# Kernel optimization log

Hardware: AMD Instinct MI355X
Metric: run time of the kernel (lower is better)

The kernel has to match this reference:

```python
import jax, jax.numpy as jnp
import numpy as np

TEMPERATURE = 0.1
GAMMA = 0.5
LOSS_WEIGHT = 1.0
N, D = 8192, 64
EPS_COS = 1e-8
EPS_NCE = 1e-6
SQ_EPS = 1e-12  # (1e-6 distance)^2


def setup_inputs() -> dict:
    key = jax.random.key(0)
    k1, k2, k3 = jax.random.split(key, 3)
    features = jax.random.normal(k1, (N, D), dtype=jnp.float32)
    labels = jax.random.randint(k2, (N,), 0, 3, dtype=jnp.int64)
    coords = jax.random.uniform(k3, (N, 3), dtype=jnp.float32)
    return {"features": features, "labels": labels, "coords": coords}


def reference(features, labels, coords):
    # line-point mask (label == 2); pairwise math on the masked subset is
    # expressed as full pairwise + (m_i & m_j) masking, mathematically
    # identical to extract-then-pairwise in the torch original.
    m = labels == 2                       # [N] bool
    mf = m.astype(features.dtype)
    L = jnp.sum(mf)                       # number of line points

    # cosine similarity: normalize then GEMM (== F.cosine_similarity pairwise)
    norm = jnp.maximum(jnp.linalg.norm(features, axis=1, keepdims=True), EPS_COS)
    fn = features / norm
    feat_sim = fn @ fn.T                  # [N, N]

    # squared pairwise coordinate distances (cdist^2), clamped >= 0
    sq_norm = jnp.sum(coords * coords, axis=1)
    sq = sq_norm[:, None] + sq_norm[None, :] - 2.0 * (coords @ coords.T)
    sq = jnp.maximum(sq, 0.0)             # [N, N]

    pair = m[:, None] & m[None, :]
    within = (sq < 1.0) & (sq > SQ_EPS)   # dist < 1.0 and dist > 1e-6
    pos = pair & within
    neg = pair & ~within                  # original neg_mask = ~pos over subset

    posf = pos.astype(feat_sim.dtype)
    negf = neg.astype(feat_sim.dtype)

    exp_sim = jnp.exp(feat_sim / TEMPERATURE)
    sum_exp = jnp.sum(exp_sim * negf, axis=1)
    pos_sum = jnp.sum(exp_sim * posf, axis=1)
    ratio = pos_sum / (sum_exp + pos_sum + EPS_NCE)
    # mean of -log(ratio) over line points only (guard non-line rows)
    per_point = -jnp.log(jnp.where(m, ratio, 1.0))
    info_nce = jnp.sum(per_point * mf) / L

    # continuity: mean over the L x L subset matrix of |(1 - sim) - dist| * pos
    safe_sq = jnp.where(pos, sq, 1.0)     # avoid sqrt(0) NaN grads on masked entries
    coord_dist = jnp.sqrt(safe_sq)
    continuity = jnp.sum(jnp.abs((1.0 - feat_sim) - coord_dist) * posf) / (L * L)

    return (info_nce + GAMMA * continuity) * LOSS_WEIGHT
```

## Files before the change

### kernel.cpp

```cpp
#include <hip/hip_runtime.h>
#include <math.h>


typedef short s16x8 __attribute__((ext_vector_type(8)));
typedef float f32x4 __attribute__((ext_vector_type(4)));

#define NPTS 8192
#define DIM 64
#define BT 128
#define GRID_P 512
#define PSTRIDE 4096
#define MAXSLOT 32

#define OFF_L 0
#define OFF_IDX 1024
#define OFF_FH (OFF_IDX + NPTS * 4)
#define OFF_FL (OFF_FH + NPTS * DIM * 2)
#define OFF_CS (OFF_FL + NPTS * DIM * 2)
#define OFF_DF (OFF_CS + NPTS * 16)
#define OFF_PP (OFF_DF + NPTS * 4)
#define OFF_PN (OFF_PP + MAXSLOT * PSTRIDE * 4)
#define OFF_CT (OFF_PN + MAXSLOT * PSTRIDE * 4)

__global__ __launch_bounds__(1024) void k_scan(const int* __restrict__ labels,
                                               int* __restrict__ idx,
                                               int* __restrict__ Lout) {
  __shared__ int wres[16];
  __shared__ int wsum[16];
  const int t = threadIdx.x;
  const int lane = t & 63;
  const int wid = t >> 6;
  const int base = t * 8;
  int w[8];
#pragma unroll
  for (int j = 0; j < 8; j++) w[j] = labels[base + j];
  int oddz = (w[1] == 0) && (w[3] == 0) && (w[5] == 0) && (w[7] == 0);
  unsigned long long wa = __ballot(!oddz);
  if (lane == 0) wres[wid] = (wa == 0ull);
  __syncthreads();
  int is64 = 1;
#pragma unroll
  for (int i = 0; i < 16; i++) is64 &= wres[i];

  int bits = 0, cnt = 0;
  if (is64) {
    const long long* l64 = (const long long*)labels;
#pragma unroll
    for (int j = 0; j < 8; j++) {
      bool f = (l64[base + j] == 2ll);
      bits |= ((int)f) << j;
      cnt += (int)f;
    }
  } else {
#pragma unroll
    for (int j = 0; j < 8; j++) {
      bool f = (w[j] == 2);
      bits |= ((int)f) << j;
      cnt += (int)f;
    }
  }
  int inc = cnt;
#pragma unroll
  for (int m = 1; m < 64; m <<= 1) {
    int v = __shfl_up(inc, m);
    if (lane >= m) inc += v;
  }
  if (lane == 63) wsum[wid] = inc;
  __syncthreads();
  if (t < 16) {
    int v = wsum[t];
    int sc = v;
#pragma unroll
    for (int m = 1; m < 16; m <<= 1) {
      int u = __shfl_up(sc, m);
      if (t >= m) sc += u;
    }
    wsum[t] = sc - v;
    if (t == 15) *Lout = sc;
  }
  __syncthreads();
  int pos = wsum[wid] + inc - cnt;
#pragma unroll
  for (int j = 0; j < 8; j++) {
    if (bits & (1 << j)) idx[pos++] = base + j;
  }
}

__global__ __launch_bounds__(256) void k_gather(const float* __restrict__ feats,
                                                const float* __restrict__ coords,
                                                const int* __restrict__ idx,
                                                const int* __restrict__ Lp,
                                                ushort* __restrict__ fnHi,
                                                ushort* __restrict__ fnLo,
                                                float4* __restrict__ cs,
                                                int* __restrict__ diagf) {
  const int L = *Lp;
  const int gw = (int)((blockIdx.x * blockDim.x + threadIdx.x) >> 6);
  const int lane = threadIdx.x & 63;
  if (gw >= L) {
    fnHi[gw * 64 + lane] = 0;
    fnLo[gw * 64 + lane] = 0;
    if (lane == 0) {
      cs[gw] = make_float4(0.f, 0.f, 0.f, 0.f);
      diagf[gw] = 0;
    }
    return;
  }
  const int row = idx[gw];
  float f = feats[row * DIM + lane];
  float ss = f * f;
#pragma unroll
  for (int m = 32; m; m >>= 1) ss += __shfl_xor(ss, m);
  float nrm = fmaxf(sqrtf(ss), 1e-8f);
  float fn = f / nrm;
  unsigned u = __float_as_uint(fn);
  unsigned hb = (u + 0x7FFFu + ((u >> 16) & 1u)) >> 16;
  float hif = __uint_as_float(hb << 16);
  float lof = fn - hif;
  unsigned ul = __float_as_uint(lof);
  unsigned lb = (ul + 0x7FFFu + ((ul >> 16) & 1u)) >> 16;
  fnHi[gw * 64 + lane] = (ushort)hb;
  fnLo[gw * 64 + lane] = (ushort)lb;
  if (lane == 0) {
    float c0 = coords[row * 3 + 0];
    float c1 = coords[row * 3 + 1];
    float c2 = coords[row * 3 + 2];
    float p0 = __fmul_rn(c0, c0);
    float p1 = __fmul_rn(c1, c1);
    float p2 = __fmul_rn(c2, c2);
    float s = __fadd_rn(__fadd_rn(p0, p1), p2);
    float g = __fadd_rn(__fadd_rn(p0, p2), p1);
    diagf[gw] = (__fadd_rn(s, -g) > 5e-13f) ? 1 : 0;
    cs[gw] = make_float4(c0, c1, c2, c0 * c0 + c1 * c1 + c2 * c2);
  }
}

__global__ __launch_bounds__(256, 3) void k_pair(const ushort* __restrict__ fnHi,
                                                 const ushort* __restrict__ fnLo,
                                                 const float4* __restrict__ cs,
                                                 const int* __restrict__ Lp,
                                                 const int* __restrict__ diagf,
                                                 float* __restrict__ pp,
                                                 float* __restrict__ pn,
                                                 float* __restrict__ contp) {
  __shared__ __attribute__((aligned(16))) ushort AB[4][128][40];
  __shared__ float cred[4];

  const int L = *Lp;
  const int nT = (L + BT - 1) >> 7;
  const int nItems = nT * nT;
  const int t = threadIdx.x;
  const int lane = t & 63, wid = t >> 6;
  const int m = lane & 15;
  const int koct = lane >> 4;
  float cont = 0.f;

  for (int wi = blockIdx.x; wi < nItems; wi += GRID_P) {
    const int bi = wi / nT;
    const int jt = wi - bi * nT;
    const bool isDiag = (bi == jt);
    const int rb = bi << 7, cb = jt << 7;

    f32x4 acc[2][8];
#pragma unroll
    for (int rt = 0; rt < 2; rt++)
#pragma unroll
      for (int ct = 0; ct < 8; ct++) acc[rt][ct] = (f32x4){0.f, 0.f, 0.f, 0.f};

#pragma unroll
    for (int kk = 0; kk < 2; kk++) {
      __syncthreads();
#pragma unroll
      for (int i = 0; i < 8; i++) {
        int q = t + 256 * i;
        int sel = q >> 9;
        int row = (q >> 2) & 127;
        int oct = q & 3;
        int slot = ((sel < 2) ? rb : cb) + row;
        const ushort* src = (sel & 1) ? fnLo : fnHi;
        s16x8 v = *(const s16x8*)&src[slot * 64 + kk * 32 + oct * 8];
        *(s16x8*)&AB[sel][row][oct * 8] = v;
      }
      __syncthreads();

      const int kofd = koct * 8;
      s16x8 ah[2], al[2], bh[8], bl[8];
#pragma unroll
      for (int rt = 0; rt < 2; rt++) {
        ah[rt] = *(const s16x8*)&AB[0][wid * 32 + rt * 16 + m][kofd];
        al[rt] = *(const s16x8*)&AB[1][wid * 32 + rt * 16 + m][kofd];
      }
#pragma unroll
      for (int ct = 0; ct < 8; ct++) {
        bh[ct] = *(const s16x8*)&AB[2][ct * 16 + m][kofd];
        bl[ct] = *(const s16x8*)&AB[3][ct * 16 + m][kofd];
      }
#pragma unroll
      for (int rt = 0; rt < 2; rt++)
#pragma unroll
        for (int ct = 0; ct < 8; ct++) {
          acc[rt][ct] = __builtin_amdgcn_mfma_f32_16x16x32_bf16(ah[rt], bh[ct], acc[rt][ct], 0, 0, 0);
          acc[rt][ct] = __builtin_amdgcn_mfma_f32_16x16x32_bf16(ah[rt], bl[ct], acc[rt][ct], 0, 0, 0);
          acc[rt][ct] = __builtin_amdgcn_mfma_f32_16x16x32_bf16(al[rt], bh[ct], acc[rt][ct], 0, 0, 0);
        }
    }

    float4 crow[2][4];
    int dfr[2][4];
#pragma unroll
    for (int rt = 0; rt < 2; rt++)
#pragma unroll
      for (int rg = 0; rg < 4; rg++) {
        int ig = rb + wid * 32 + rt * 16 + koct * 4 + rg;
        crow[rt][rg] = cs[ig];
        dfr[rt][rg] = isDiag ? diagf[ig] : 0;
      }
    float pos_r[2][4] = {{0.f, 0.f, 0.f, 0.f}, {0.f, 0.f, 0.f, 0.f}};
    float neg_r[2][4] = {{0.f, 0.f, 0.f, 0.f}, {0.f, 0.f, 0.f, 0.f}};
#pragma unroll
    for (int ct = 0; ct < 8; ct++) {
      int jg = cb + ct * 16 + m;
      float4 cbv = cs[jg];
      bool jv = (jg < L);
#pragma unroll
      for (int rt = 0; rt < 2; rt++)
#pragma unroll
        for (int rg = 0; rg < 4; rg++) {
          int ig = rb + wid * 32 + rt * 16 + koct * 4 + rg;
          bool valid = jv && (ig < L);
          float sim = acc[rt][ct][rg];
          float4 cav = crow[rt][rg];
          float d3 = cav.x * cbv.x + cav.y * cbv.y + cav.z * cbv.z;
          float sq = fmaxf(cav.w + cbv.w - 2.f * d3, 0.f);
          bool within = (sq < 1.0f) && (sq > 1e-12f);
          if (isDiag && ig == jg) within = (dfr[rt][rg] != 0);
          float e = __expf(sim * 10.f);
          if (valid) {
            if (within) {
              pos_r[rt][rg] += e;
              cont += fabsf(1.f - sim - sqrtf(sq));
            } else {
              neg_r[rt][rg] += e;
            }
          }
        }
    }
#pragma unroll
    for (int rt = 0; rt < 2; rt++)
#pragma unroll
      for (int rg = 0; rg < 4; rg++) {
        float p = pos_r[rt][rg], n = neg_r[rt][rg];
#pragma unroll
        for (int s1 = 1; s1 < 16; s1 <<= 1) {
          p += __shfl_xor(p, s1);
          n += __shfl_xor(n, s1);
        }
        if (m == 0) {
          int ig = rb + wid * 32 + rt * 16 + koct * 4 + rg;
          pp[jt * PSTRIDE + ig] = p;
          pn[jt * PSTRIDE + ig] = n;
        }
      }
  }

#pragma unroll
  for (int s1 = 1; s1 < 64; s1 <<= 1) cont += __shfl_xor(cont, s1);
  __syncthreads();
  if (lane == 0) cred[wid] = cont;
  __syncthreads();
  if (t == 0) contp[blockIdx.x] = cred[0] + cred[1] + cred[2] + cred[3];
}

__global__ __launch_bounds__(1024) void k_final(const float* __restrict__ pp,
                                                const float* __restrict__ pn,
                                                const float* __restrict__ contp,
                                                const int* __restrict__ Lp,
                                                float* __restrict__ out) {
  __shared__ float red[32];
  const int L = *Lp;
  const int nslots = (L + BT - 1) >> 7;
  const int t = threadIdx.x;
  float accI = 0.f;
  for (int s = t; s < L; s += 1024) {
    float pos = 0.f, neg = 0.f;
    for (int c = 0; c < nslots; c++) {
      pos += pp[c * PSTRIDE + s];
      neg += pn[c * PSTRIDE + s];
    }
    accI += -logf(pos / (neg + pos + 1e-6f));
  }
  float accC = 0.f;
  for (int c = t; c < GRID_P; c += 1024) accC += contp[c];
#pragma unroll
  for (int m = 1; m < 64; m <<= 1) {
    accI += __shfl_xor(accI, m);
    accC += __shfl_xor(accC, m);
  }
  if ((t & 63) == 0) {
    red[t >> 6] = accI;
    red[16 + (t >> 6)] = accC;
  }
  __syncthreads();
  if (t == 0) {
    float sI = 0.f, sC = 0.f;
#pragma unroll
    for (int w = 0; w < 16; w++) {
      sI += red[w];
      sC += red[16 + w];
    }
    float fL = (float)L;
    out[0] = sI / fL + 0.5f * (sC / (fL * fL));
  }
}

extern "C" void kernel_launch(void* const* d_in, const int* in_sizes, int n_in,
                              void* d_out, int out_size, void* d_ws, size_t ws_size,
                              hipStream_t stream) {
  const float* features = (const float*)d_in[0];
  const int* labels = (const int*)d_in[1];
  const float* coords = (const float*)d_in[2];

  char* ws = (char*)d_ws;
  int* Lp = (int*)(ws + OFF_L);
  int* idx = (int*)(ws + OFF_IDX);
  ushort* fnHi = (ushort*)(ws + OFF_FH);
  ushort* fnLo = (ushort*)(ws + OFF_FL);
  float4* cs = (float4*)(ws + OFF_CS);
  int* diagf = (int*)(ws + OFF_DF);
  float* pp = (float*)(ws + OFF_PP);
  float* pn = (float*)(ws + OFF_PN);
  float* contp = (float*)(ws + OFF_CT);
  float* out = (float*)d_out;

  k_scan<<<1, 1024, 0, stream>>>(labels, idx, Lp);
  k_gather<<<(NPTS * 64) / 256, 256, 0, stream>>>(features, coords, idx, Lp, fnHi, fnLo, cs, diagf);
  k_pair<<<GRID_P, 256, 0, stream>>>(fnHi, fnLo, cs, Lp, diagf, pp, pn, contp);
  k_final<<<1, 1024, 0, stream>>>(pp, pn, contp, Lp, out);
}
```

Before: 49.84 us.

## Fuse label scan and feature gather into one multi-block prep kernel

Merges the single-block label compaction scan and the per-row normalize/split gather into one kernel. Each of 64 blocks redundantly recomputes the prefix scan into shared memory and then gathers its share of rows, which removes a kernel launch and the global index buffer. In exchange, the scan is redundant across blocks and uses a barrier-heavy shared-memory Hillis-Steele loop. The gather also runs with far fewer blocks, and padding now stops at the next multiple of 128 rather than covering all rows.

```diff
diff --git a/kernel.cpp b/kernel.cpp
--- a/kernel.cpp
+++ b/kernel.cpp
@@ -13,8 +13,7 @@
 #define MAXSLOT 32
 
 #define OFF_L 0
-#define OFF_IDX 1024
-#define OFF_FH (OFF_IDX + NPTS * 4)
+#define OFF_FH 1024
 #define OFF_FL (OFF_FH + NPTS * DIM * 2)
 #define OFF_CS (OFF_FL + NPTS * DIM * 2)
 #define OFF_DF (OFF_CS + NPTS * 16)
@@ -22,15 +21,22 @@
 #define OFF_PN (OFF_PP + MAXSLOT * PSTRIDE * 4)
 #define OFF_CT (OFF_PN + MAXSLOT * PSTRIDE * 4)
 
-__global__ __launch_bounds__(1024) void k_scan(const int* __restrict__ labels,
-                                               int* __restrict__ idx,
-                                               int* __restrict__ Lout) {
+__global__ __launch_bounds__(1024) void k_prep(const float* __restrict__ feats,
+                                               const int* __restrict__ labels,
+                                               const float* __restrict__ coords,
+                                               int* __restrict__ Lp,
+                                               ushort* __restrict__ fnHi,
+                                               ushort* __restrict__ fnLo,
+                                               float4* __restrict__ cs,
+                                               int* __restrict__ diagf) {
+  __shared__ int sc[1024];
+  __shared__ int sidx[NPTS];
   __shared__ int wres[16];
-  __shared__ int wsum[16];
   const int t = threadIdx.x;
   const int lane = t & 63;
   const int wid = t >> 6;
   const int base = t * 8;
+
   int w[8];
 #pragma unroll
   for (int j = 0; j < 8; j++) w[j] = labels[base + j];
@@ -59,79 +65,62 @@
       cnt += (int)f;
     }
   }
-  int inc = cnt;
-#pragma unroll
-  for (int m = 1; m < 64; m <<= 1) {
-    int v = __shfl_up(inc, m);
-    if (lane >= m) inc += v;
-  }
-  if (lane == 63) wsum[wid] = inc;
-  __syncthreads();
-  if (t < 16) {
-    int v = wsum[t];
-    int sc = v;
-#pragma unroll
-    for (int m = 1; m < 16; m <<= 1) {
-      int u = __shfl_up(sc, m);
-      if (t >= m) sc += u;
-    }
-    wsum[t] = sc - v;
-    if (t == 15) *Lout = sc;
-  }
-  __syncthreads();
-  int pos = wsum[wid] + inc - cnt;
+  sc[t] = cnt;
+  __syncthreads();
+  for (int off = 1; off < 1024; off <<= 1) {
+    int v = 0;
+    if (t >= off) v = sc[t - off];
+    __syncthreads();
+    sc[t] += v;
+    __syncthreads();
+  }
+  int pos = sc[t] - cnt;
 #pragma unroll
   for (int j = 0; j < 8; j++) {
-    if (bits & (1 << j)) idx[pos++] = base + j;
-  }
-}
-
-__global__ __launch_bounds__(256) void k_gather(const float* __restrict__ feats,
-                                                const float* __restrict__ coords,
-                                                const int* __restrict__ idx,
-                                                const int* __restrict__ Lp,
-                                                ushort* __restrict__ fnHi,
-                                                ushort* __restrict__ fnLo,
-                                                float4* __restrict__ cs,
-                                                int* __restrict__ diagf) {
-  const int L = *Lp;
-  const int gw = (int)((blockIdx.x * blockDim.x + threadIdx.x) >> 6);
-  const int lane = threadIdx.x & 63;
-  if (gw >= L) {
-    fnHi[gw * 64 + lane] = 0;
-    fnLo[gw * 64 + lane] = 0;
-    if (lane == 0) {
-      cs[gw] = make_float4(0.f, 0.f, 0.f, 0.f);
-      diagf[gw] = 0;
-    }
-    return;
-  }
-  const int row = idx[gw];
-  float f = feats[row * DIM + lane];
-  float ss = f * f;
-#pragma unroll
-  for (int m = 32; m; m >>= 1) ss += __shfl_xor(ss, m);
-  float nrm = fmaxf(sqrtf(ss), 1e-8f);
-  float fn = f / nrm;
-  unsigned u = __float_as_uint(fn);
-  unsigned hb = (u + 0x7FFFu + ((u >> 16) & 1u)) >> 16;
-  float hif = __uint_as_float(hb << 16);
-  float lof = fn - hif;
-  unsigned ul = __float_as_uint(lof);
-  unsigned lb = (ul + 0x7FFFu + ((ul >> 16) & 1u)) >> 16;
-  fnHi[gw * 64 + lane] = (ushort)hb;
-  fnLo[gw * 64 + lane] = (ushort)lb;
-  if (lane == 0) {
-    float c0 = coords[row * 3 + 0];
-    float c1 = coords[row * 3 + 1];
-    float c2 = coords[row * 3 + 2];
-    float p0 = __fmul_rn(c0, c0);
-    float p1 = __fmul_rn(c1, c1);
-    float p2 = __fmul_rn(c2, c2);
-    float s = __fadd_rn(__fadd_rn(p0, p1), p2);
-    float g = __fadd_rn(__fadd_rn(p0, p2), p1);
-    diagf[gw] = (__fadd_rn(s, -g) > 5e-13f) ? 1 : 0;
-    cs[gw] = make_float4(c0, c1, c2, c0 * c0 + c1 * c1 + c2 * c2);
+    if (bits & (1 << j)) sidx[pos++] = base + j;
+  }
+  __syncthreads();
+  const int L = sc[1023];
+  if (blockIdx.x == 0 && t == 0) *Lp = L;
+  const int Lpad = (L + 127) & ~127;
+
+  for (int slot = (int)blockIdx.x * 16 + wid; slot < Lpad; slot += 64 * 16) {
+    if (slot < L) {
+      const int row = sidx[slot];
+      float f = feats[row * DIM + lane];
+      float ss = f * f;
+#pragma unroll
+      for (int m1 = 32; m1; m1 >>= 1) ss += __shfl_xor(ss, m1);
+      float nrm = fmaxf(sqrtf(ss), 1e-8f);
+      float fn = f / nrm;
+      unsigned u = __float_as_uint(fn);
+      unsigned hb = (u + 0x7FFFu + ((u >> 16) & 1u)) >> 16;
+      float hif = __uint_as_float(hb << 16);
+      float lof = fn - hif;
+      unsigned ul = __float_as_uint(lof);
+      unsigned lb = (ul + 0x7FFFu + ((ul >> 16) & 1u)) >> 16;
+      fnHi[slot * 64 + lane] = (ushort)hb;
+      fnLo[slot * 64 + lane] = (ushort)lb;
+      if (lane == 0) {
+        float c0 = coords[row * 3 + 0];
+        float c1 = coords[row * 3 + 1];
+        float c2 = coords[row * 3 + 2];
+        float p0 = __fmul_rn(c0, c0);
+        float p1 = __fmul_rn(c1, c1);
+        float p2 = __fmul_rn(c2, c2);
+        float s_ = __fadd_rn(__fadd_rn(p0, p1), p2);
+        float g_ = __fadd_rn(__fadd_rn(p0, p2), p1);
+        diagf[slot] = (__fadd_rn(s_, -g_) > 5e-13f) ? 1 : 0;
+        cs[slot] = make_float4(c0, c1, c2, c0 * c0 + c1 * c1 + c2 * c2);
+      }
+    } else {
+      fnHi[slot * 64 + lane] = 0;
+      fnLo[slot * 64 + lane] = 0;
+      if (lane == 0) {
+        cs[slot] = make_float4(0.f, 0.f, 0.f, 0.f);
+        diagf[slot] = 0;
+      }
+    }
   }
 }
 
@@ -322,7 +311,6 @@
 
   char* ws = (char*)d_ws;
   int* Lp = (int*)(ws + OFF_L);
-  int* idx = (int*)(ws + OFF_IDX);
   ushort* fnHi = (ushort*)(ws + OFF_FH);
   ushort* fnLo = (ushort*)(ws + OFF_FL);
   float4* cs = (float4*)(ws + OFF_CS);
@@ -332,8 +320,8 @@
   float* contp = (float*)(ws + OFF_CT);
   float* out = (float*)d_out;
 
-  k_scan<<<1, 1024, 0, stream>>>(labels, idx, Lp);
-  k_gather<<<(NPTS * 64) / 256, 256, 0, stream>>>(features, coords, idx, Lp, fnHi, fnLo, cs, diagf);
+  k_prep<<<64, 1024, 0, stream>>>(features, labels, coords, Lp, fnHi, fnLo,
+                                  cs, diagf);
   k_pair<<<GRID_P, 256, 0, stream>>>(fnHi, fnLo, cs, Lp, diagf, pp, pn, contp);
   k_final<<<1, 1024, 0, stream>>>(pp, pn, contp, Lp, out);
 }
```

After: 49.23 us. About the same (-1.2%).
